# Performance work log

Measured on AMD Instinct MI355X. Metric: run time of the kernel, lower is better.

The kernel has to match this reference:

```python
import jax, jax.numpy as jnp
import numpy as np
from jax import lax

B, S, F, K = 64, 256, 8, 4
D = F + 6          # mem_sequence_dim = 14
FLAT = 32 * 15 * 15  # vision flatten dim for 64x64 input


def _linear(x, w, b):
    return x @ w.T + b


def _conv(x, w, b, pad):
    y = lax.conv_general_dilated(x, w, (1, 1), pad, dimension_numbers=('NCHW', 'OIHW', 'NCHW'))
    return y + b[None, :, None, None]


def _avgpool2(x):
    return lax.reduce_window(x, 0.0, lax.add, (1, 1, 2, 2), (1, 1, 2, 2), 'VALID') * 0.25


def _ln(x, g, b):
    m = x.mean(-1, keepdims=True)
    v = ((x - m) ** 2).mean(-1, keepdims=True)
    return (x - m) / jnp.sqrt(v + 1e-5) * g + b


def setup_inputs() -> dict:
    key = jax.random.key(0)
    ks = jax.random.split(key, 40)
    p = lambda i, shape, s=0.1: jax.random.normal(ks[i], shape, jnp.float32) * s
    return {
        'x': jax.random.uniform(ks[0], (B, 3, 64, 64), jnp.float32),
        'conv1_w': p(1, (16, 3, 3, 3)), 'conv1_b': jnp.zeros((16,), jnp.float32),
        'conv2_w': p(2, (32, 16, 3, 3)), 'conv2_b': jnp.zeros((32,), jnp.float32),
        'conv3_w': p(3, (32, 32, 3, 3)), 'conv3_b': jnp.zeros((32,), jnp.float32),
        'venc_w': p(4, (F, FLAT), 0.02), 'venc_b': jnp.zeros((F,), jnp.float32),
        'tenc1_w': p(5, (64, 3)), 'tenc1_b': jnp.zeros((64,), jnp.float32),
        'tenc2_w': p(6, (D, 64)), 'tenc2_b': jnp.zeros((D,), jnp.float32),
        'attn_in_w': p(7, (3 * D, D)), 'attn_in_b': jnp.zeros((3 * D,), jnp.float32),
        'attn_out_w': p(8, (D, D)), 'attn_out_b': jnp.zeros((D,), jnp.float32),
        'ln1_g': jnp.ones((D,), jnp.float32), 'ln1_b': jnp.zeros((D,), jnp.float32),
        'ln2_g': jnp.ones((D,), jnp.float32), 'ln2_b': jnp.zeros((D,), jnp.float32),
        'ffn1_w': p(9, (2 * D, D)), 'ffn1_b': jnp.zeros((2 * D,), jnp.float32),
        'ffn2_w': p(10, (D, 2 * D)), 'ffn2_b': jnp.zeros((D,), jnp.float32),
        'head1_w': p(11, (512, 2 * D)), 'head1_b': jnp.zeros((512,), jnp.float32),
        'head2_w': p(12, (128, 512)), 'head2_b': jnp.zeros((128,), jnp.float32),
        'head3_w': p(13, (6, 128)), 'head3_b': jnp.zeros((6,), jnp.float32),
        'mem_nodes': jax.random.normal(ks[14], (B, S, F), jnp.float32),
        'mem_edges': jax.random.uniform(ks[15], (B, S, S, 6), jnp.float32) * 10.0,
    }


def reference(x, conv1_w, conv1_b, conv2_w, conv2_b, conv3_w, conv3_b, venc_w, venc_b,
              tenc1_w, tenc1_b, tenc2_w, tenc2_b, attn_in_w, attn_in_b, attn_out_w, attn_out_b,
              ln1_g, ln1_b, ln2_g, ln2_b, ffn1_w, ffn1_b, ffn2_w, ffn2_b,
              head1_w, head1_b, head2_w, head2_b, head3_w, head3_b, mem_nodes, mem_edges):
    Bc = x.shape[0]
    # target color encoding from top-left pixel
    target_color = x[:, :, 0, 0]                                    # (B,3)
    t = jax.nn.relu(_linear(target_color, tenc1_w, tenc1_b))
    target_enc = _linear(t, tenc2_w, tenc2_b)[:, None, :]           # (B,1,D)
    # vision CNN
    h = x - 0.5
    h = jax.nn.relu(_avgpool2(_conv(h, conv1_w, conv1_b, 'VALID')))          # (B,16,31,31)
    h = jax.nn.relu(_avgpool2(_conv(h, conv2_w, conv2_b, [(1, 1), (1, 1)]))) # (B,32,15,15)
    h = jax.nn.relu(_conv(h, conv3_w, conv3_b, [(1, 1), (1, 1)]))            # (B,32,15,15)
    vision_enc = _linear(h.reshape(Bc, -1), venc_w, venc_b)         # (B,F)
    # closest memory node (Euclidean cdist + argmin)
    dists = jnp.linalg.norm(vision_enc[:, None, :] - mem_nodes, axis=-1)  # (B,S)
    closest = jnp.argmin(dists, axis=1)                             # (B,)
    # min-over-actions transition cost, then Bellman-Ford SSSP (S-1 relaxations)
    cost = mem_edges.min(axis=-1)                                   # (B,S,S)
    bidx = jnp.arange(Bc)
    d0 = cost[bidx, closest, :].at[bidx, closest].set(0.0)          # (B,S)

    def body(d, _):
        d = jnp.minimum(d, jnp.min(d[:, :, None] + cost, axis=1))
        return d, None

    d, _ = lax.scan(body, d0, None, length=S - 1)
    spd = jnp.where(jnp.isinf(d), 1e9, d)
    _, topk_idx = lax.top_k(-spd, K)                                # (B,K) closest-by-path
    # retrieve node features and min outgoing edge costs
    retrieved_nodes = jnp.take_along_axis(mem_nodes, topk_idx[:, :, None], axis=1)  # (B,K,F)
    min_out = mem_edges.min(axis=2)                                 # (B,S,6)
    retrieved_edges = jnp.take_along_axis(min_out, topk_idx[:, :, None], axis=1)    # (B,K,6)
    seq = jnp.concatenate([target_enc, jnp.concatenate([retrieved_nodes, retrieved_edges], -1)], axis=1)  # (B,1+K,D)
    # one post-norm transformer encoder layer (nhead=1, relu, eval/no-dropout)
    qkv = _linear(seq, attn_in_w, attn_in_b)
    q, k_, v = jnp.split(qkv, 3, axis=-1)
    attn = jax.nn.softmax(jnp.einsum('bqd,bkd->bqk', q, k_) / jnp.sqrt(jnp.float32(D)), axis=-1)
    ctx = _linear(jnp.einsum('bqk,bkd->bqd', attn, v), attn_out_w, attn_out_b)
    seq = _ln(seq + ctx, ln1_g, ln1_b)
    ff = _linear(jax.nn.relu(_linear(seq, ffn1_w, ffn1_b)), ffn2_w, ffn2_b)
    seq = _ln(seq + ff, ln2_g, ln2_b)
    # head on [target ctx ; mean memory ctx]
    h2 = jnp.concatenate([seq[:, 0], seq[:, 1:].mean(axis=1)], axis=-1)  # (B,2D)
    h2 = jax.nn.relu(_linear(h2, head1_w, head1_b))
    h2 = jax.nn.relu(_linear(h2, head2_w, head2_b))
    return _linear(h2, head3_w, head3_b)                            # (B,6) Q-values
```

## Files before the change

kernel.cpp:

```cpp
#include <hip/hip_runtime.h>
#include <math.h>

#define BB 64

static __device__ __forceinline__ float relu_(float v){ return v > 0.f ? v : 0.f; }

static __device__ void cost_body(const float* __restrict__ edges, float* __restrict__ cost,
                                 float* __restrict__ minout, int bi, float* red) {
    int j = threadIdx.x;
    const float* e = edges + ((size_t)bi * 256 + j) * 6;
    float m0 = e[0], m1 = e[1], m2 = e[2], m3 = e[3], m4 = e[4], m5 = e[5];
    cost[(size_t)bi * 256 + j] = fminf(fminf(fminf(m0, m1), fminf(m2, m3)), fminf(m4, m5));
    red[0*256+j]=m0; red[1*256+j]=m1; red[2*256+j]=m2;
    red[3*256+j]=m3; red[4*256+j]=m4; red[5*256+j]=m5;
    __syncthreads();
    for (int st = 128; st > 0; st >>= 1) {
        if (j < st) {
            #pragma unroll
            for (int q = 0; q < 6; ++q) red[q*256+j] = fminf(red[q*256+j], red[q*256+j+st]);
        }
        __syncthreads();
    }
    if (j < 6) minout[(size_t)bi * 6 + j] = red[j*256];
}

#define C1_BLOCKS 128
__global__ __launch_bounds__(256) void k_conv1(const float* __restrict__ x, const float* __restrict__ w,
        const float* __restrict__ bias, float* __restrict__ h1,
        const float* __restrict__ edges, float* __restrict__ cost, float* __restrict__ minout, int costBase) {
    __shared__ float sm[2210 + 6435 + 432 + 16];
    if ((int)blockIdx.x >= C1_BLOCKS) {
        int bi = costBase + (int)blockIdx.x - C1_BLOCKS;
        if (bi < BB * 256) cost_body(edges, cost, minout, bi, sm);
        return;
    }
    float* iBuf = sm; float* T = sm + 2210; float* sW = T + 6435; float* sB = sW + 432;
    int b = blockIdx.x >> 1, rg = blockIdx.x & 1;
    int t = threadIdx.x;
    int nyo = rg ? 15 : 16;
    int r0 = rg * 16, rowbase = rg * 32;
    int nrows = rg ? 32 : 34;
    for (int i = t; i < 432; i += 256) sW[i] = w[i];
    if (t < 16) sB[t] = bias[t];
    int na = 2 * nyo + 1;
    for (int ci = 0; ci < 3; ++ci) {
        __syncthreads();
        int tot = nrows * 64;
        for (int e = t; e < tot; e += 256) {
            int r = e >> 6, c = e & 63;
            iBuf[r * 65 + c] = x[(size_t)b * 12288 + ci * 4096 + (rowbase + r) * 64 + c] - 0.5f;
        }
        __syncthreads();
        int tot2 = na * 63;
        for (int e2 = t; e2 < tot2; e2 += 256) {
            int a = e2 / 63, c = e2 % 63;
            float* p = iBuf + a * 65 + c;
            T[ci * 2145 + a * 65 + c] = (p[0] + p[1]) + (p[65] + p[66]);
        }
    }
    __syncthreads();
    int npos = 31 * nyo;
    int p1 = t + 256;
    int yo0 = t / 31, xo0 = t % 31;
    bool v1 = p1 < npos;
    int yo1 = v1 ? p1 / 31 : 0, xo1 = v1 ? p1 % 31 : 0;
    float acc0[16], acc1[16];
    #pragma unroll
    for (int o = 0; o < 16; ++o) { acc0[o] = 0.f; acc1[o] = 0.f; }
    #pragma unroll 1
    for (int ci = 0; ci < 3; ++ci) {
        const float* T0 = T + ci * 2145 + yo0 * 130 + xo0 * 2;
        const float* T1 = T + ci * 2145 + yo1 * 130 + xo1 * 2;
        #pragma unroll
        for (int ky = 0; ky < 3; ++ky)
        #pragma unroll
        for (int kx = 0; kx < 3; ++kx) {
            float s0 = T0[ky * 65 + kx], s1 = T1[ky * 65 + kx];
            #pragma unroll
            for (int o = 0; o < 16; ++o) {
                float wv = sW[o * 27 + ci * 9 + ky * 3 + kx];
                acc0[o] += s0 * wv; acc1[o] += s1 * wv;
            }
        }
    }
    size_t ob = (size_t)b * 15376;
    #pragma unroll
    for (int o = 0; o < 16; ++o) {
        h1[ob + o * 961 + (r0 + yo0) * 31 + xo0] = relu_(0.25f * acc0[o] + sB[o]);
        if (v1) h1[ob + o * 961 + (r0 + yo1) * 31 + xo1] = relu_(0.25f * acc1[o] + sB[o]);
    }
}

#define C2_BLOCKS 256
__global__ __launch_bounds__(256) void k_conv2(const float* __restrict__ h1, const float* __restrict__ w,
        const float* __restrict__ bias, float* __restrict__ h2,
        const float* __restrict__ edges, float* __restrict__ cost, float* __restrict__ minout, int costBase) {
    __shared__ float sm[1024 + 16368 + 1152 + 8];
    if ((int)blockIdx.x >= C2_BLOCKS) {
        int bi = costBase + (int)blockIdx.x - C2_BLOCKS;
        if (bi < BB * 256) cost_body(edges, cost, minout, bi, sm);
        return;
    }
    float* iBuf = sm; float* T = sm + 1024; float* sW = T + 16368; float* sB = sW + 1152;
    int b = blockIdx.x >> 2, og = blockIdx.x & 3;
    int t = threadIdx.x;
    for (int i = t; i < 1152; i += 256) sW[i] = w[og * 1152 + i];
    if (t < 8) sB[t] = bias[og * 8 + t];
    for (int ci = 0; ci < 16; ++ci) {
        __syncthreads();
        for (int e = t; e < 1024; e += 256) {
            int r = e >> 5, c = e & 31;
            int iy = r - 1, ix = c - 1;
            float v = 0.f;
            if (iy >= 0 && iy < 31 && ix >= 0 && ix < 31)
                v = h1[(size_t)b * 15376 + ci * 961 + iy * 31 + ix];
            iBuf[e] = v;
        }
        __syncthreads();
        for (int e = t; e < 961; e += 256) {
            int a = e / 31, c = e % 31;
            float* p = iBuf + a * 32 + c;
            T[ci * 1023 + a * 33 + c] = (p[0] + p[1]) + (p[32] + p[33]);
        }
    }
    __syncthreads();
    if (t < 225) {
        int yo = t / 15, xo = t % 15;
        float acc[8];
        #pragma unroll
        for (int o = 0; o < 8; ++o) acc[o] = 0.f;
        #pragma unroll 1
        for (int ci = 0; ci < 16; ++ci) {
            const float* Tp = T + ci * 1023 + yo * 66 + xo * 2;
            #pragma unroll
            for (int ky = 0; ky < 3; ++ky)
            #pragma unroll
            for (int kx = 0; kx < 3; ++kx) {
                float s = Tp[ky * 33 + kx];
                #pragma unroll
                for (int o = 0; o < 8; ++o) acc[o] += s * sW[o * 144 + ci * 9 + ky * 3 + kx];
            }
        }
        size_t ob = (size_t)b * 7200 + (og * 8) * 225 + t;
        #pragma unroll
        for (int o = 0; o < 8; ++o) h2[ob + o * 225] = relu_(0.25f * acc[o] + sB[o]);
    }
}

#define C3_BLOCKS 256
__global__ __launch_bounds__(256) void k_conv3(const float* __restrict__ h2, const float* __restrict__ w,
        const float* __restrict__ bias, float* __restrict__ h3,
        const float* __restrict__ edges, float* __restrict__ cost, float* __restrict__ minout, int costBase) {
    __shared__ float sm[9248 + 2304 + 8];
    if ((int)blockIdx.x >= C3_BLOCKS) {
        int bi = costBase + (int)blockIdx.x - C3_BLOCKS;
        if (bi < BB * 256) cost_body(edges, cost, minout, bi, sm);
        return;
    }
    float* sIn = sm; float* sW = sm + 9248; float* sB = sW + 2304;
    int b = blockIdx.x >> 2, og = blockIdx.x & 3;
    int t = threadIdx.x;
    for (int i = t; i < 2304; i += 256) sW[i] = w[og * 2304 + i];
    if (t < 8) sB[t] = bias[og * 8 + t];
    for (int e = t; e < 9248; e += 256) {
        int ci = e / 289, rem = e % 289;
        int r = rem / 17, c = rem % 17;
        int iy = r - 1, ix = c - 1;
        float v = 0.f;
        if (iy >= 0 && iy < 15 && ix >= 0 && ix < 15)
            v = h2[(size_t)b * 7200 + ci * 225 + iy * 15 + ix];
        sIn[e] = v;
    }
    __syncthreads();
    if (t < 225) {
        int yo = t / 15, xo = t % 15;
        float acc[8];
        #pragma unroll
        for (int o = 0; o < 8; ++o) acc[o] = 0.f;
        #pragma unroll 1
        for (int ci = 0; ci < 32; ++ci) {
            const float* Ip = sIn + ci * 289 + yo * 17 + xo;
            const float* Wp = sW + ci * 9;
            #pragma unroll
            for (int ky = 0; ky < 3; ++ky)
            #pragma unroll
            for (int kx = 0; kx < 3; ++kx) {
                float iv = Ip[ky * 17 + kx];
                #pragma unroll
                for (int o = 0; o < 8; ++o) acc[o] += iv * Wp[o * 288 + ky * 3 + kx];
            }
        }
        size_t ob = (size_t)b * 7200 + (og * 8) * 225 + t;
        #pragma unroll
        for (int o = 0; o < 8; ++o) h3[ob + o * 225] = relu_(acc[o] + sB[o]);
    }
}

__global__ __launch_bounds__(1024, 4) void k_bellman(
        const float* __restrict__ h3, const float* __restrict__ vew, const float* __restrict__ veb,
        const float* __restrict__ nodes, const float* __restrict__ cost, float* __restrict__ dout) {
    int b = blockIdx.x; int tid = threadIdx.x;
    __shared__ float vred[1024];
    __shared__ float ve_s[8];
    __shared__ float val[256]; __shared__ int idx[256];
    __shared__ __align__(16) float d_lds[256];
    __shared__ __align__(16) float part[1024];

    {
        int f = tid >> 7, i = tid & 127;
        const float* hb = h3 + (size_t)b * 7200;
        const float* wf = vew + (size_t)f * 7200;
        float s = 0.f;
        for (int k = i; k < 7200; k += 128) s += hb[k] * wf[k];
        vred[tid] = s; __syncthreads();
        for (int st = 64; st > 0; st >>= 1) {
            if (i < st) vred[tid] += vred[tid + st];
            __syncthreads();
        }
        if (i == 0) ve_s[f] = vred[tid] + veb[f];
        __syncthreads();
    }
    if (tid < 256) {
        const float* n = nodes + ((size_t)b * 256 + tid) * 8;
        float acc = 0.f;
        #pragma unroll
        for (int f = 0; f < 8; ++f) { float df = ve_s[f] - n[f]; acc += df * df; }
        val[tid] = acc; idx[tid] = tid;
    }
    __syncthreads();
    for (int st = 128; st > 0; st >>= 1) {
        if (tid < st) {
            float ov = val[tid + st]; int oi = idx[tid + st];
            if (ov < val[tid] || (ov == val[tid] && oi < idx[tid])) { val[tid] = ov; idx[tid] = oi; }
        }
        __syncthreads();
    }
    int src = idx[0];
    int jg = tid >> 8, t = tid & 255;
    const float* cb = cost + (size_t)b * 65536;
    float creg[64];
    #pragma unroll
    for (int jj = 0; jj < 64; ++jj)
        creg[jj] = cb[(size_t)((jg << 6) | jj) * 256 + t];
    float dv = 0.f;
    if (jg == 0) {
        dv = (t == src) ? 0.f : cb[(size_t)src * 256 + t];
        d_lds[t] = dv;
    }
    __syncthreads();
    for (int it = 0; it < 255; ++it) {
        float p = 3.402823466e+38f;
        const float4* d4 = (const float4*)(d_lds + (jg << 6));
        #pragma unroll
        for (int q = 0; q < 16; ++q) {
            float4 dd = d4[q];
            p = fminf(p, fminf(fminf(dd.x + creg[4*q+0], dd.y + creg[4*q+1]),
                               fminf(dd.z + creg[4*q+2], dd.w + creg[4*q+3])));
        }
        part[(jg << 8) | t] = p;
        __syncthreads();
        int ch = 0;
        if (jg == 0) {
            float m = fminf(fminf(part[t], part[256 + t]), fminf(part[512 + t], part[768 + t]));
            float nd = fminf(dv, m);
            ch = nd < dv;
            dv = nd;
            d_lds[t] = nd;
        }
        if (__syncthreads_count(ch) == 0) break;
    }
    if (jg == 0) dout[(size_t)b * 256 + t] = dv;
}

__global__ void k_head(const float* __restrict__ x,
                       const float* __restrict__ w1, const float* __restrict__ b1,
                       const float* __restrict__ w2, const float* __restrict__ b2,
                       const float* __restrict__ dvec, const float* __restrict__ nodes,
                       const float* __restrict__ minout,
                       const float* __restrict__ Wi, const float* __restrict__ bi_,
                       const float* __restrict__ Wo, const float* __restrict__ bo,
                       const float* __restrict__ g1, const float* __restrict__ be1,
                       const float* __restrict__ g2, const float* __restrict__ be2,
                       const float* __restrict__ W1, const float* __restrict__ bf1,
                       const float* __restrict__ W2, const float* __restrict__ bf2,
                       const float* __restrict__ H1, const float* __restrict__ hb1,
                       const float* __restrict__ H2, const float* __restrict__ hb2,
                       const float* __restrict__ H3, const float* __restrict__ hb3,
                       float* __restrict__ out) {
    int b = blockIdx.x, t = threadIdx.x;
    __shared__ float sq[70], qkv[210], sc[25], tmp[70], f1[140], h2c[28];
    __shared__ __align__(16) float a1[512];
    __shared__ float part[256]; __shared__ float a2[128];
    __shared__ float tc[3]; __shared__ float tt[64];
    __shared__ float val[256]; __shared__ int idx[256]; __shared__ int sel[4];

    if (t < 3) tc[t] = x[(size_t)b * 12288 + t * 4096];
    __syncthreads();
    if (t < 64) tt[t] = relu_(b1[t] + tc[0] * w1[t * 3] + tc[1] * w1[t * 3 + 1] + tc[2] * w1[t * 3 + 2]);
    __syncthreads();
    if (t < 14) {
        float e = b2[t];
        for (int o = 0; o < 64; ++o) e += tt[o] * w2[t * 64 + o];
        sq[t] = e;
    }
    float dv = dvec[(size_t)b * 256 + t];
    if (isinf(dv)) dv = 1e9f;
    float myv = dv;
    for (int k = 0; k < 4; ++k) {
        val[t] = myv; idx[t] = t; __syncthreads();
        for (int st = 128; st > 0; st >>= 1) {
            if (t < st) {
                float ov = val[t + st]; int oi = idx[t + st];
                if (ov < val[t] || (ov == val[t] && oi < idx[t])) { val[t] = ov; idx[t] = oi; }
            }
            __syncthreads();
        }
        if (t == 0) sel[k] = idx[0];
        __syncthreads();
        if (t == sel[k]) myv = 3.402823466e+38f;
    }
    if (t >= 64 && t < 64 + 56) {
        int u = t - 64; int k = u / 14; int c = u % 14; int id_ = sel[k];
        sq[(1 + k) * 14 + c] = (c < 8) ? nodes[((size_t)b * 256 + id_) * 8 + c]
                                       : minout[((size_t)b * 256 + id_) * 6 + (c - 8)];
    }
    __syncthreads();

    if (t < 210) {
        int r = t / 42, o = t % 42; float v = bi_[o];
        for (int dd = 0; dd < 14; ++dd) v += sq[r * 14 + dd] * Wi[o * 14 + dd];
        qkv[t] = v;
    }
    __syncthreads();
    if (t < 25) {
        int r = t / 5, c = t % 5; float v = 0.f;
        for (int dd = 0; dd < 14; ++dd) v += qkv[r * 42 + dd] * qkv[c * 42 + 14 + dd];
        sc[t] = v / sqrtf(14.0f);
    }
    __syncthreads();
    if (t < 5) {
        float mx = sc[t * 5];
        for (int c = 1; c < 5; ++c) mx = fmaxf(mx, sc[t * 5 + c]);
        float e[5]; float sm = 0.f;
        for (int c = 0; c < 5; ++c) { e[c] = expf(sc[t * 5 + c] - mx); sm += e[c]; }
        for (int c = 0; c < 5; ++c) sc[t * 5 + c] = e[c] / sm;
    }
    __syncthreads();
    if (t < 70) {
        int r = t / 14, dd = t % 14; float v = 0.f;
        for (int c = 0; c < 5; ++c) v += sc[r * 5 + c] * qkv[c * 42 + 28 + dd];
        tmp[t] = v;
    }
    __syncthreads();
    if (t < 70) {
        int r = t / 14, o = t % 14; float v = bo[o];
        for (int dd = 0; dd < 14; ++dd) v += tmp[r * 14 + dd] * Wo[o * 14 + dd];
        f1[t] = sq[t] + v;
    }
    __syncthreads();
    if (t < 5) {
        float m = 0.f; for (int dd = 0; dd < 14; ++dd) m += f1[t * 14 + dd]; m /= 14.f;
        float v = 0.f; for (int dd = 0; dd < 14; ++dd) { float z = f1[t * 14 + dd] - m; v += z * z; } v /= 14.f;
        float inv = 1.f / sqrtf(v + 1e-5f);
        for (int dd = 0; dd < 14; ++dd) sq[t * 14 + dd] = (f1[t * 14 + dd] - m) * inv * g1[dd] + be1[dd];
    }
    __syncthreads();
    if (t < 140) {
        int r = t / 28, o = t % 28; float v = bf1[o];
        for (int dd = 0; dd < 14; ++dd) v += sq[r * 14 + dd] * W1[o * 14 + dd];
        f1[t] = relu_(v);
    }
    __syncthreads();
    if (t < 70) {
        int r = t / 14, o = t % 14; float v = bf2[o];
        for (int i = 0; i < 28; ++i) v += f1[r * 28 + i] * W2[o * 28 + i];
        tmp[t] = sq[t] + v;
    }
    __syncthreads();
    if (t < 5) {
        float m = 0.f; for (int dd = 0; dd < 14; ++dd) m += tmp[t * 14 + dd]; m /= 14.f;
        float v = 0.f; for (int dd = 0; dd < 14; ++dd) { float z = tmp[t * 14 + dd] - m; v += z * z; } v /= 14.f;
        float inv = 1.f / sqrtf(v + 1e-5f);
        for (int dd = 0; dd < 14; ++dd) sq[t * 14 + dd] = (tmp[t * 14 + dd] - m) * inv * g2[dd] + be2[dd];
    }
    __syncthreads();
    if (t < 28) {
        int c = t - 14;
        h2c[t] = (t < 14) ? sq[t]
                          : 0.25f * (sq[14 + c] + sq[28 + c] + sq[42 + c] + sq[56 + c]);
    }
    __syncthreads();
    {
        #pragma unroll
        for (int rep = 0; rep < 2; ++rep) {
            int o = t + rep * 256;
            const float4* Hr = (const float4*)(H1 + o * 28);
            float v = hb1[o];
            #pragma unroll
            for (int i = 0; i < 7; ++i) {
                float4 h4 = Hr[i];
                v += h4.x * h2c[i*4] + h4.y * h2c[i*4+1] + h4.z * h2c[i*4+2] + h4.w * h2c[i*4+3];
            }
            a1[o] = relu_(v);
        }
    }
    __syncthreads();
    {
        int o = t & 127, half = t >> 7;
        const float4* Hr = (const float4*)(H2 + o * 512 + half * 256);
        const float* ap = a1 + half * 256;
        float v = 0.f;
        for (int i = 0; i < 64; ++i) {
            float4 h4 = Hr[i];
            v += h4.x * ap[i*4] + h4.y * ap[i*4+1] + h4.z * ap[i*4+2] + h4.w * ap[i*4+3];
        }
        part[t] = v;
    }
    __syncthreads();
    if (t < 128) a2[t] = relu_(hb2[t] + part[t] + part[t + 128]);
    __syncthreads();
    if (t < 6) {
        const float4* Hr = (const float4*)(H3 + t * 128);
        float v = hb3[t];
        for (int i = 0; i < 32; ++i) {
            float4 h4 = Hr[i];
            v += h4.x * a2[i*4] + h4.y * a2[i*4+1] + h4.z * a2[i*4+2] + h4.w * a2[i*4+3];
        }
        out[b * 6 + t] = v;
    }
}

extern "C" void kernel_launch(void* const* d_in, const int* in_sizes, int n_in,
                              void* d_out, int out_size, void* d_ws, size_t ws_size,
                              hipStream_t stream) {
    const float* x   = (const float*)d_in[0];
    const float* c1w = (const float*)d_in[1];
    const float* c1b = (const float*)d_in[2];
    const float* c2w = (const float*)d_in[3];
    const float* c2b = (const float*)d_in[4];
    const float* c3w = (const float*)d_in[5];
    const float* c3b = (const float*)d_in[6];
    const float* vew = (const float*)d_in[7];
    const float* veb = (const float*)d_in[8];
    const float* t1w = (const float*)d_in[9];
    const float* t1b = (const float*)d_in[10];
    const float* t2w = (const float*)d_in[11];
    const float* t2b = (const float*)d_in[12];
    const float* aiw = (const float*)d_in[13];
    const float* aib = (const float*)d_in[14];
    const float* aow = (const float*)d_in[15];
    const float* aob = (const float*)d_in[16];
    const float* l1g = (const float*)d_in[17];
    const float* l1bb= (const float*)d_in[18];
    const float* l2g = (const float*)d_in[19];
    const float* l2bb= (const float*)d_in[20];
    const float* f1w = (const float*)d_in[21];
    const float* f1b = (const float*)d_in[22];
    const float* f2w = (const float*)d_in[23];
    const float* f2b = (const float*)d_in[24];
    const float* h1w = (const float*)d_in[25];
    const float* h1b = (const float*)d_in[26];
    const float* h2w = (const float*)d_in[27];
    const float* h2b = (const float*)d_in[28];
    const float* h3w = (const float*)d_in[29];
    const float* h3b = (const float*)d_in[30];
    const float* nodes = (const float*)d_in[31];
    const float* edges = (const float*)d_in[32];

    float* W = (float*)d_ws;
    float* dvec   = W + 8192;
    float* h1     = W + 32768;
    float* h2     = W + 1016832;
    float* h3     = W + 1477632;
    float* minout = W + 1938432;
    float* cost   = W + 2097152;

    const int nc1 = 5461, nc2 = 5461, nc3 = 5462;
    k_conv1<<<C1_BLOCKS + nc1, 256, 0, stream>>>(x, c1w, c1b, h1, edges, cost, minout, 0);
    k_conv2<<<C2_BLOCKS + nc2, 256, 0, stream>>>(h1, c2w, c2b, h2, edges, cost, minout, nc1);
    k_conv3<<<C3_BLOCKS + nc3, 256, 0, stream>>>(h2, c3w, c3b, h3, edges, cost, minout, nc1 + nc2);
    k_bellman<<<BB, 1024, 0, stream>>>(h3, vew, veb, nodes, cost, dvec);
    k_head<<<BB, 256, 0, stream>>>(x, t1w, t1b, t2w, t2b, dvec, nodes, minout,
                                   aiw, aib, aow, aob, l1g, l1bb, l2g, l2bb,
                                   f1w, f1b, f2w, f2b, h1w, h1b, h2w, h2b, h3w, h3b,
                                   (float*)d_out);
}
```

Measured before the change: 169.9 us.

## Fuse conv3 with vision encoder and Bellman with head; rebalance cost work

Conv3 now runs as one 1024-thread block per batch element, keeps its output in shared memory and computes the vision encoding and nearest-node argmin in the same kernel, so h3 is never written to global memory. The Bellman-Ford relaxation and the transformer/MLP head are merged into a single tail kernel, removing one launch and the round trip of the distance vector. The edge-cost min work that conv3 used to carry now goes to conv1 and conv2 only. The trade-off is that conv3 runs on just 64 blocks, which is less parallel than the previous 256 blocks plus filler work, and the heavier conv1/conv2 launches may lengthen them.

```diff
diff --git a/kernel.cpp b/kernel.cpp
--- a/kernel.cpp
+++ b/kernel.cpp
@@ -147,22 +147,18 @@
     }
 }
 
-#define C3_BLOCKS 256
-__global__ __launch_bounds__(256) void k_conv3(const float* __restrict__ h2, const float* __restrict__ w,
-        const float* __restrict__ bias, float* __restrict__ h3,
-        const float* __restrict__ edges, float* __restrict__ cost, float* __restrict__ minout, int costBase) {
-    __shared__ float sm[9248 + 2304 + 8];
-    if ((int)blockIdx.x >= C3_BLOCKS) {
-        int bi = costBase + (int)blockIdx.x - C3_BLOCKS;
-        if (bi < BB * 256) cost_body(edges, cost, minout, bi, sm);
-        return;
-    }
-    float* sIn = sm; float* sW = sm + 9248; float* sB = sW + 2304;
-    int b = blockIdx.x >> 2, og = blockIdx.x & 3;
-    int t = threadIdx.x;
-    for (int i = t; i < 2304; i += 256) sW[i] = w[og * 2304 + i];
-    if (t < 8) sB[t] = bias[og * 8 + t];
-    for (int e = t; e < 9248; e += 256) {
+__global__ __launch_bounds__(1024) void k_conv3ve(const float* __restrict__ h2, const float* __restrict__ w,
+        const float* __restrict__ bias, const float* __restrict__ vew, const float* __restrict__ veb,
+        const float* __restrict__ nodes, int* __restrict__ closest) {
+    __shared__ float sIn[9248];
+    __shared__ float sW[9216];
+    __shared__ float h3s[7200];
+    __shared__ float vred[1024];
+    __shared__ float ve_s[8];
+    __shared__ float val[256]; __shared__ int idx[256];
+    int b = blockIdx.x; int tid = threadIdx.x;
+    int og = tid >> 8, t = tid & 255;
+    for (int e = tid; e < 9248; e += 1024) {
         int ci = e / 289, rem = e % 289;
         int r = rem / 17, c = rem % 17;
         int iy = r - 1, ix = c - 1;
@@ -171,16 +167,18 @@
             v = h2[(size_t)b * 7200 + ci * 225 + iy * 15 + ix];
         sIn[e] = v;
     }
+    for (int e = tid; e < 9216; e += 1024) sW[e] = w[e];
     __syncthreads();
     if (t < 225) {
         int yo = t / 15, xo = t % 15;
         float acc[8];
         #pragma unroll
         for (int o = 0; o < 8; ++o) acc[o] = 0.f;
+        const float* Wg = sW + (og * 8) * 288;
         #pragma unroll 1
         for (int ci = 0; ci < 32; ++ci) {
             const float* Ip = sIn + ci * 289 + yo * 17 + xo;
-            const float* Wp = sW + ci * 9;
+            const float* Wp = Wg + ci * 9;
             #pragma unroll
             for (int ky = 0; ky < 3; ++ky)
             #pragma unroll
@@ -190,28 +188,16 @@
                 for (int o = 0; o < 8; ++o) acc[o] += iv * Wp[o * 288 + ky * 3 + kx];
             }
         }
-        size_t ob = (size_t)b * 7200 + (og * 8) * 225 + t;
-        #pragma unroll
-        for (int o = 0; o < 8; ++o) h3[ob + o * 225] = relu_(acc[o] + sB[o]);
-    }
-}
-
-__global__ __launch_bounds__(1024, 4) void k_bellman(
-        const float* __restrict__ h3, const float* __restrict__ vew, const float* __restrict__ veb,
-        const float* __restrict__ nodes, const float* __restrict__ cost, float* __restrict__ dout) {
-    int b = blockIdx.x; int tid = threadIdx.x;
-    __shared__ float vred[1024];
-    __shared__ float ve_s[8];
-    __shared__ float val[256]; __shared__ int idx[256];
-    __shared__ __align__(16) float d_lds[256];
-    __shared__ __align__(16) float part[1024];
-
+        #pragma unroll
+        for (int o = 0; o < 8; ++o)
+            h3s[(og * 8 + o) * 225 + t] = relu_(acc[o] + bias[og * 8 + o]);
+    }
+    __syncthreads();
     {
         int f = tid >> 7, i = tid & 127;
-        const float* hb = h3 + (size_t)b * 7200;
         const float* wf = vew + (size_t)f * 7200;
         float s = 0.f;
-        for (int k = i; k < 7200; k += 128) s += hb[k] * wf[k];
+        for (int k = i; k < 7200; k += 128) s += h3s[k] * wf[k];
         vred[tid] = s; __syncthreads();
         for (int st = 64; st > 0; st >>= 1) {
             if (i < st) vred[tid] += vred[tid + st];
@@ -235,8 +221,36 @@
         }
         __syncthreads();
     }
-    int src = idx[0];
+    if (tid == 0) closest[b] = idx[0];
+}
+
+__global__ __launch_bounds__(1024, 4) void k_tail(
+        const float* __restrict__ x, const int* __restrict__ closest,
+        const float* __restrict__ cost, const float* __restrict__ nodes,
+        const float* __restrict__ minout,
+        const float* __restrict__ w1, const float* __restrict__ b1,
+        const float* __restrict__ w2, const float* __restrict__ b2,
+        const float* __restrict__ Wi, const float* __restrict__ bi_,
+        const float* __restrict__ Wo, const float* __restrict__ bo,
+        const float* __restrict__ g1, const float* __restrict__ be1,
+        const float* __restrict__ g2, const float* __restrict__ be2,
+        const float* __restrict__ W1, const float* __restrict__ bf1,
+        const float* __restrict__ W2, const float* __restrict__ bf2,
+        const float* __restrict__ H1, const float* __restrict__ hb1,
+        const float* __restrict__ H2, const float* __restrict__ hb2,
+        const float* __restrict__ H3, const float* __restrict__ hb3,
+        float* __restrict__ out) {
+    int b = blockIdx.x; int tid = threadIdx.x;
     int jg = tid >> 8, t = tid & 255;
+    __shared__ __align__(16) float d_lds[256];
+    __shared__ __align__(16) float part_b[1024];
+    __shared__ float val[256]; __shared__ int idx[256]; __shared__ int sel[4];
+    __shared__ float tc[3]; __shared__ float tt[64];
+    __shared__ float sq[70], qkv[210], sc[25], tmp[70], f1[140], h2c[28];
+    __shared__ __align__(16) float a1[512];
+    __shared__ float parth[512]; __shared__ float a2[128];
+
+    int src = closest[b];
     const float* cb = cost + (size_t)b * 65536;
     float creg[64];
     #pragma unroll
@@ -257,11 +271,11 @@
             p = fminf(p, fminf(fminf(dd.x + creg[4*q+0], dd.y + creg[4*q+1]),
                                fminf(dd.z + creg[4*q+2], dd.w + creg[4*q+3])));
         }
-        part[(jg << 8) | t] = p;
+        part_b[(jg << 8) | t] = p;
         __syncthreads();
         int ch = 0;
         if (jg == 0) {
-            float m = fminf(fminf(part[t], part[256 + t]), fminf(part[512 + t], part[768 + t]));
+            float m = fminf(fminf(part_b[t], part_b[256 + t]), fminf(part_b[512 + t], part_b[768 + t]));
             float nd = fminf(dv, m);
             ch = nd < dv;
             dv = nd;
@@ -269,164 +283,142 @@
         }
         if (__syncthreads_count(ch) == 0) break;
     }
-    if (jg == 0) dout[(size_t)b * 256 + t] = dv;
-}
-
-__global__ void k_head(const float* __restrict__ x,
-                       const float* __restrict__ w1, const float* __restrict__ b1,
-                       const float* __restrict__ w2, const float* __restrict__ b2,
-                       const float* __restrict__ dvec, const float* __restrict__ nodes,
-                       const float* __restrict__ minout,
-                       const float* __restrict__ Wi, const float* __restrict__ bi_,
-                       const float* __restrict__ Wo, const float* __restrict__ bo,
-                       const float* __restrict__ g1, const float* __restrict__ be1,
-                       const float* __restrict__ g2, const float* __restrict__ be2,
-                       const float* __restrict__ W1, const float* __restrict__ bf1,
-                       const float* __restrict__ W2, const float* __restrict__ bf2,
-                       const float* __restrict__ H1, const float* __restrict__ hb1,
-                       const float* __restrict__ H2, const float* __restrict__ hb2,
-                       const float* __restrict__ H3, const float* __restrict__ hb3,
-                       float* __restrict__ out) {
-    int b = blockIdx.x, t = threadIdx.x;
-    __shared__ float sq[70], qkv[210], sc[25], tmp[70], f1[140], h2c[28];
-    __shared__ __align__(16) float a1[512];
-    __shared__ float part[256]; __shared__ float a2[128];
-    __shared__ float tc[3]; __shared__ float tt[64];
-    __shared__ float val[256]; __shared__ int idx[256]; __shared__ int sel[4];
-
-    if (t < 3) tc[t] = x[(size_t)b * 12288 + t * 4096];
-    __syncthreads();
-    if (t < 64) tt[t] = relu_(b1[t] + tc[0] * w1[t * 3] + tc[1] * w1[t * 3 + 1] + tc[2] * w1[t * 3 + 2]);
-    __syncthreads();
-    if (t < 14) {
-        float e = b2[t];
-        for (int o = 0; o < 64; ++o) e += tt[o] * w2[t * 64 + o];
-        sq[t] = e;
-    }
-    float dv = dvec[(size_t)b * 256 + t];
-    if (isinf(dv)) dv = 1e9f;
-    float myv = dv;
+
+    if (tid < 3) tc[tid] = x[(size_t)b * 12288 + tid * 4096];
+    __syncthreads();
+    if (tid < 64) tt[tid] = relu_(b1[tid] + tc[0] * w1[tid * 3] + tc[1] * w1[tid * 3 + 1] + tc[2] * w1[tid * 3 + 2]);
+    __syncthreads();
+    if (tid < 14) {
+        float e = b2[tid];
+        for (int o = 0; o < 64; ++o) e += tt[o] * w2[tid * 64 + o];
+        sq[tid] = e;
+    }
+    float myv = 0.f;
+    if (tid < 256) {
+        float dvv = d_lds[tid];
+        if (isinf(dvv)) dvv = 1e9f;
+        myv = dvv;
+    }
     for (int k = 0; k < 4; ++k) {
-        val[t] = myv; idx[t] = t; __syncthreads();
+        if (tid < 256) { val[tid] = myv; idx[tid] = tid; }
+        __syncthreads();
         for (int st = 128; st > 0; st >>= 1) {
-            if (t < st) {
-                float ov = val[t + st]; int oi = idx[t + st];
-                if (ov < val[t] || (ov == val[t] && oi < idx[t])) { val[t] = ov; idx[t] = oi; }
+            if (tid < st) {
+                float ov = val[tid + st]; int oi = idx[tid + st];
+                if (ov < val[tid] || (ov == val[tid] && oi < idx[tid])) { val[tid] = ov; idx[tid] = oi; }
             }
             __syncthreads();
         }
-        if (t == 0) sel[k] = idx[0];
-        __syncthreads();
-        if (t == sel[k]) myv = 3.402823466e+38f;
-    }
-    if (t >= 64 && t < 64 + 56) {
-        int u = t - 64; int k = u / 14; int c = u % 14; int id_ = sel[k];
+        if (tid == 0) sel[k] = idx[0];
+        __syncthreads();
+        if (tid < 256 && tid == sel[k]) myv = 3.402823466e+38f;
+    }
+    if (tid >= 64 && tid < 64 + 56) {
+        int u = tid - 64; int k = u / 14; int c = u % 14; int id_ = sel[k];
         sq[(1 + k) * 14 + c] = (c < 8) ? nodes[((size_t)b * 256 + id_) * 8 + c]
                                        : minout[((size_t)b * 256 + id_) * 6 + (c - 8)];
     }
     __syncthreads();
 
-    if (t < 210) {
-        int r = t / 42, o = t % 42; float v = bi_[o];
+    if (tid < 210) {
+        int r = tid / 42, o = tid % 42; float v = bi_[o];
         for (int dd = 0; dd < 14; ++dd) v += sq[r * 14 + dd] * Wi[o * 14 + dd];
-        qkv[t] = v;
-    }
-    __syncthreads();
-    if (t < 25) {
-        int r = t / 5, c = t % 5; float v = 0.f;
+        qkv[tid] = v;
+    }
+    __syncthreads();
+    if (tid < 25) {
+        int r = tid / 5, c = tid % 5; float v = 0.f;
         for (int dd = 0; dd < 14; ++dd) v += qkv[r * 42 + dd] * qkv[c * 42 + 14 + dd];
-        sc[t] = v / sqrtf(14.0f);
-    }
-    __syncthreads();
-    if (t < 5) {
-        float mx = sc[t * 5];
-        for (int c = 1; c < 5; ++c) mx = fmaxf(mx, sc[t * 5 + c]);
+        sc[tid] = v / sqrtf(14.0f);
+    }
+    __syncthreads();
+    if (tid < 5) {
+        float mx = sc[tid * 5];
+        for (int c = 1; c < 5; ++c) mx = fmaxf(mx, sc[tid * 5 + c]);
         float e[5]; float sm = 0.f;
-        for (int c = 0; c < 5; ++c) { e[c] = expf(sc[t * 5 + c] - mx); sm += e[c]; }
-        for (int c = 0; c < 5; ++c) sc[t * 5 + c] = e[c] / sm;
-    }
-    __syncthreads();
-    if (t < 70) {
-        int r = t / 14, dd = t % 14; float v = 0.f;
+        for (int c = 0; c < 5; ++c) { e[c] = expf(sc[tid * 5 + c] - mx); sm += e[c]; }
+        for (int c = 0; c < 5; ++c) sc[tid * 5 + c] = e[c] / sm;
+    }
+    __syncthreads();
+    if (tid < 70) {
+        int r = tid / 14, dd = tid % 14; float v = 0.f;
         for (int c = 0; c < 5; ++c) v += sc[r * 5 + c] * qkv[c * 42 + 28 + dd];
-        tmp[t] = v;
-    }
-    __syncthreads();
-    if (t < 70) {
-        int r = t / 14, o = t % 14; float v = bo[o];
+        tmp[tid] = v;
+    }
+    __syncthreads();
+    if (tid < 70) {
+        int r = tid / 14, o = tid % 14; float v = bo[o];
         for (int dd = 0; dd < 14; ++dd) v += tmp[r * 14 + dd] * Wo[o * 14 + dd];
-        f1[t] = sq[t] + v;
-    }
-    __syncthreads();
-    if (t < 5) {
-        float m = 0.f; for (int dd = 0; dd < 14; ++dd) m += f1[t * 14 + dd]; m /= 14.f;
-        float v = 0.f; for (int dd = 0; dd < 14; ++dd) { float z = f1[t * 14 + dd] - m; v += z * z; } v /= 14.f;
+        f1[tid] = sq[tid] + v;
+    }
+    __syncthreads();
+    if (tid < 5) {
+        float m = 0.f; for (int dd = 0; dd < 14; ++dd) m += f1[tid * 14 + dd]; m /= 14.f;
+        float v = 0.f; for (int dd = 0; dd < 14; ++dd) { float z = f1[tid * 14 + dd] - m; v += z * z; } v /= 14.f;
         float inv = 1.f / sqrtf(v + 1e-5f);
-        for (int dd = 0; dd < 14; ++dd) sq[t * 14 + dd] = (f1[t * 14 + dd] - m) * inv * g1[dd] + be1[dd];
-    }
-    __syncthreads();
-    if (t < 140) {
-        int r = t / 28, o = t % 28; float v = bf1[o];
+        for (int dd = 0; dd < 14; ++dd) sq[tid * 14 + dd] = (f1[tid * 14 + dd] - m) * inv * g1[dd] + be1[dd];
+    }
+    __syncthreads();
+    if (tid < 140) {
+        int r = tid / 28, o = tid % 28; float v = bf1[o];
         for (int dd = 0; dd < 14; ++dd) v += sq[r * 14 + dd] * W1[o * 14 + dd];
-        f1[t] = relu_(v);
-    }
-    __syncthreads();
-    if (t < 70) {
-        int r = t / 14, o = t % 14; float v = bf2[o];
+        f1[tid] = relu_(v);
+    }
+    __syncthreads();
+    if (tid < 70) {
+        int r = tid / 14, o = tid % 14; float v = bf2[o];
         for (int i = 0; i < 28; ++i) v += f1[r * 28 + i] * W2[o * 28 + i];
-        tmp[t] = sq[t] + v;
-    }
-    __syncthreads();
-    if (t < 5) {
-        float m = 0.f; for (int dd = 0; dd < 14; ++dd) m += tmp[t * 14 + dd]; m /= 14.f;
-        float v = 0.f; for (int dd = 0; dd < 14; ++dd) { float z = tmp[t * 14 + dd] - m; v += z * z; } v /= 14.f;
+        tmp[tid] = sq[tid] + v;
+    }
+    __syncthreads();
+    if (tid < 5) {
+        float m = 0.f; for (int dd = 0; dd < 14; ++dd) m += tmp[tid * 14 + dd]; m /= 14.f;
+        float v = 0.f; for (int dd = 0; dd < 14; ++dd) { float z = tmp[tid * 14 + dd] - m; v += z * z; } v /= 14.f;
         float inv = 1.f / sqrtf(v + 1e-5f);
-        for (int dd = 0; dd < 14; ++dd) sq[t * 14 + dd] = (tmp[t * 14 + dd] - m) * inv * g2[dd] + be2[dd];
-    }
-    __syncthreads();
-    if (t < 28) {
-        int c = t - 14;
-        h2c[t] = (t < 14) ? sq[t]
-                          : 0.25f * (sq[14 + c] + sq[28 + c] + sq[42 + c] + sq[56 + c]);
-    }
-    __syncthreads();
-    {
-        #pragma unroll
-        for (int rep = 0; rep < 2; ++rep) {
-            int o = t + rep * 256;
-            const float4* Hr = (const float4*)(H1 + o * 28);
-            float v = hb1[o];
-            #pragma unroll
-            for (int i = 0; i < 7; ++i) {
-                float4 h4 = Hr[i];
-                v += h4.x * h2c[i*4] + h4.y * h2c[i*4+1] + h4.z * h2c[i*4+2] + h4.w * h2c[i*4+3];
-            }
-            a1[o] = relu_(v);
-        }
-    }
-    __syncthreads();
-    {
-        int o = t & 127, half = t >> 7;
-        const float4* Hr = (const float4*)(H2 + o * 512 + half * 256);
-        const float* ap = a1 + half * 256;
+        for (int dd = 0; dd < 14; ++dd) sq[tid * 14 + dd] = (tmp[tid * 14 + dd] - m) * inv * g2[dd] + be2[dd];
+    }
+    __syncthreads();
+    if (tid < 28) {
+        int c = tid - 14;
+        h2c[tid] = (tid < 14) ? sq[tid]
+                              : 0.25f * (sq[14 + c] + sq[28 + c] + sq[42 + c] + sq[56 + c]);
+    }
+    __syncthreads();
+    if (tid < 512) {
+        int o = tid;
+        const float4* Hr = (const float4*)(H1 + o * 28);
+        float v = hb1[o];
+        #pragma unroll
+        for (int i = 0; i < 7; ++i) {
+            float4 h4 = Hr[i];
+            v += h4.x * h2c[i*4] + h4.y * h2c[i*4+1] + h4.z * h2c[i*4+2] + h4.w * h2c[i*4+3];
+        }
+        a1[o] = relu_(v);
+    }
+    __syncthreads();
+    if (tid < 512) {
+        int o = tid & 127, q = tid >> 7;
+        const float4* Hr = (const float4*)(H2 + o * 512 + q * 128);
+        const float* ap = a1 + q * 128;
         float v = 0.f;
-        for (int i = 0; i < 64; ++i) {
+        #pragma unroll
+        for (int i = 0; i < 32; ++i) {
             float4 h4 = Hr[i];
             v += h4.x * ap[i*4] + h4.y * ap[i*4+1] + h4.z * ap[i*4+2] + h4.w * ap[i*4+3];
         }
-        part[t] = v;
-    }
-    __syncthreads();
-    if (t < 128) a2[t] = relu_(hb2[t] + part[t] + part[t + 128]);
-    __syncthreads();
-    if (t < 6) {
-        const float4* Hr = (const float4*)(H3 + t * 128);
-        float v = hb3[t];
+        parth[tid] = v;
+    }
+    __syncthreads();
+    if (tid < 128) a2[tid] = relu_(hb2[tid] + parth[tid] + parth[tid + 128] + parth[tid + 256] + parth[tid + 384]);
+    __syncthreads();
+    if (tid < 6) {
+        const float4* Hr = (const float4*)(H3 + tid * 128);
+        float v = hb3[tid];
         for (int i = 0; i < 32; ++i) {
             float4 h4 = Hr[i];
             v += h4.x * a2[i*4] + h4.y * a2[i*4+1] + h4.z * a2[i*4+2] + h4.w * a2[i*4+3];
         }
-        out[b * 6 + t] = v;
+        out[b * 6 + tid] = v;
     }
 }
 
@@ -468,20 +460,19 @@
     const float* edges = (const float*)d_in[32];
 
     float* W = (float*)d_ws;
-    float* dvec   = W + 8192;
+    int*   closest = (int*)(W + 512);
     float* h1     = W + 32768;
     float* h2     = W + 1016832;
-    float* h3     = W + 1477632;
     float* minout = W + 1938432;
     float* cost   = W + 2097152;
 
-    const int nc1 = 5461, nc2 = 5461, nc3 = 5462;
+    const int nc1 = 8192, nc2 = 8192;
     k_conv1<<<C1_BLOCKS + nc1, 256, 0, stream>>>(x, c1w, c1b, h1, edges, cost, minout, 0);
     k_conv2<<<C2_BLOCKS + nc2, 256, 0, stream>>>(h1, c2w, c2b, h2, edges, cost, minout, nc1);
-    k_conv3<<<C3_BLOCKS + nc3, 256, 0, stream>>>(h2, c3w, c3b, h3, edges, cost, minout, nc1 + nc2);
-    k_bellman<<<BB, 1024, 0, stream>>>(h3, vew, veb, nodes, cost, dvec);
-    k_head<<<BB, 256, 0, stream>>>(x, t1w, t1b, t2w, t2b, dvec, nodes, minout,
-                                   aiw, aib, aow, aob, l1g, l1bb, l2g, l2bb,
-                                   f1w, f1b, f2w, f2b, h1w, h1b, h2w, h2b, h3w, h3b,
-                                   (float*)d_out);
-}
+    k_conv3ve<<<BB, 1024, 0, stream>>>(h2, c3w, c3b, vew, veb, nodes, closest);
+    k_tail<<<BB, 1024, 0, stream>>>(x, closest, cost, nodes, minout,
+                                    t1w, t1b, t2w, t2b,
+                                    aiw, aib, aow, aob, l1g, l1bb, l2g, l2bb,
+                                    f1w, f1b, f2w, f2b, h1w, h1b, h2w, h2b, h3w, h3b,
+                                    (float*)d_out);
+}
```

New measurement: 197.2 us. +16.0%, slower.
